# Performance work log

Measured on AMD Instinct MI355X. Metric: run time of the kernel, lower is better.

## Reference

```python
import jax, jax.numpy as jnp
import numpy as np

T, H, E, I, TOP_K = 4096, 1024, 8, 2048, 2
EPS = 1e-05


def setup_inputs() -> dict:
    key = jax.random.key(0)
    ks = jax.random.split(key, 4)
    x = jax.random.normal(ks[0], (T, H), dtype=jnp.float32)
    scale = jnp.ones((H,), dtype=jnp.float32)
    gate_kernel = jax.random.normal(ks[1], (H, E), dtype=jnp.float32) * (1.0 / np.sqrt(H))
    gate_bias = jnp.zeros((E,), dtype=jnp.float32)
    mlp1_weight = jax.random.normal(ks[2], (E, H, 2 * I), dtype=jnp.float32) * (1.0 / np.sqrt(H))
    mlp1_bias = jnp.zeros((E, 2 * I), dtype=jnp.float32)
    mlp2_weight = jax.random.normal(ks[3], (E, I, H), dtype=jnp.float32) * (1.0 / np.sqrt(I))
    mlp2_bias = jnp.zeros((E, H), dtype=jnp.float32)
    return {"x": x, "scale": scale, "gate_kernel": gate_kernel, "gate_bias": gate_bias,
            "mlp1_weight": mlp1_weight, "mlp1_bias": mlp1_bias,
            "mlp2_weight": mlp2_weight, "mlp2_bias": mlp2_bias}


def _rmsnorm(x, scale):
    t = x.astype(jnp.float32)
    rms = jnp.sqrt(jnp.mean(t * t, axis=-1, keepdims=True) + EPS)
    return ((t / rms) * scale).astype(x.dtype)


def reference(x, scale, gate_kernel, gate_bias, mlp1_weight, mlp1_bias, mlp2_weight, mlp2_bias):
    normed = _rmsnorm(x, scale)                                   # [T, H]
    _ = normed @ gate_kernel + gate_bias                          # gate logits (unused: static routing)
    # dense per-token, all-expert MLP: [T,H] x [E,H,2I] -> [T,E,2I]
    hidden = jnp.einsum('th,ehi->tei', normed, mlp1_weight) + mlp1_bias
    gate = jnp.minimum(hidden[..., :I], 7.0)
    linear = jnp.clip(hidden[..., I:], -7.0, 7.0)
    activated = gate * jax.nn.sigmoid(1.702 * gate) * (linear + 1.0)
    expert_out = jnp.einsum('tei,eih->teh', activated, mlp2_weight) + mlp2_bias  # [T,E,H]
    # static uniform routing over the first TOP_K experts
    mix = jnp.where(jnp.arange(E) < TOP_K, 1.0 / TOP_K, 0.0).astype(x.dtype)     # [E]
    fused = jnp.einsum('teh,e->th', expert_out, mix)
    return x + fused
```

## Files before the change

kernel.cpp:

```cpp
#include <hip/hip_runtime.h>
#include <hip/hip_bf16.h>
#include <stdint.h>

#define T_DIM 4096
#define H_DIM 1024
#define I_DIM 2048

typedef __bf16 bf16x8 __attribute__((ext_vector_type(8)));
typedef float f32x4 __attribute__((ext_vector_type(4)));
typedef unsigned short ushort_t;
typedef unsigned short us4 __attribute__((ext_vector_type(4)));

__device__ __forceinline__ unsigned short f32_to_bf16(float f) {
  unsigned int u = __float_as_uint(f);
  u += 0x7fffu + ((u >> 16) & 1u);
  return (unsigned short)(u >> 16);
}

__device__ __forceinline__ void gload_lds16(const void* g, void* l) {
  __builtin_amdgcn_global_load_lds(
      (__attribute__((address_space(1))) void*)(uintptr_t)g,
      (__attribute__((address_space(3))) void*)(unsigned int)(uintptr_t)l,
      16, 0, 0);
}

__device__ __forceinline__ int swz(int L) { return L ^ (((L >> 7) & 7) << 4); }

#define S_BARRIER() asm volatile("s_barrier" ::: "memory")
#define WAITV(n) asm volatile("s_waitcnt vmcnt(" #n ")" ::: "memory")
#define IRFENCE() asm volatile("" ::: "memory")
#define MFMA16(acc, va, vb) \
  acc = __builtin_amdgcn_mfma_f32_16x16x32_bf16(va, vb, acc, 0, 0, 0)

__global__ __launch_bounds__(256) void k_rmsnorm_init(
    const float* __restrict__ x, const float* __restrict__ scale,
    const float* __restrict__ b2, ushort_t* __restrict__ normed,
    float* __restrict__ out) {
  const int row = blockIdx.x, tid = threadIdx.x;
  const float4 v = ((const float4*)(x + (size_t)row * H_DIM))[tid];
  float ss = v.x * v.x + v.y * v.y + v.z * v.z + v.w * v.w;
#pragma unroll
  for (int off = 32; off > 0; off >>= 1) ss += __shfl_xor(ss, off);
  __shared__ float wsum[4];
  if ((tid & 63) == 0) wsum[tid >> 6] = ss;
  __syncthreads();
  const float tot = wsum[0] + wsum[1] + wsum[2] + wsum[3];
  const float inv = rsqrtf(tot * (1.0f / H_DIM) + 1e-5f);
  const float4 sc = ((const float4*)scale)[tid];
  us4 o;
  o.x = f32_to_bf16(v.x * inv * sc.x);
  o.y = f32_to_bf16(v.y * inv * sc.y);
  o.z = f32_to_bf16(v.z * inv * sc.z);
  o.w = f32_to_bf16(v.w * inv * sc.w);
  ((us4*)(normed + (size_t)row * H_DIM))[tid] = o;
  const float4 b0 = ((const float4*)b2)[tid];
  const float4 b1 = ((const float4*)(b2 + H_DIM))[tid];
  float4 ov;
  ov.x = v.x + 0.5f * (b0.x + b1.x);
  ov.y = v.y + 0.5f * (b0.y + b1.y);
  ov.z = v.z + 0.5f * (b0.z + b1.z);
  ov.w = v.w + 0.5f * (b0.w + b1.w);
  ((float4*)(out + (size_t)row * H_DIM))[tid] = ov;
}

__global__ __launch_bounds__(256) void k_transpose_cvt(const float* __restrict__ src,
                                                       ushort_t* __restrict__ dst,
                                                       int R, int C) {
  __shared__ float tile[32][33];
  const size_t eoff = (size_t)blockIdx.z * (size_t)R * (size_t)C;
  src += eoff;
  dst += eoff;
  const int x0 = blockIdx.x * 32, y0 = blockIdx.y * 32;
  const int tx = threadIdx.x & 31, ty = threadIdx.x >> 5;
#pragma unroll
  for (int i = 0; i < 4; ++i)
    tile[ty + 8 * i][tx] = src[(size_t)(y0 + ty + 8 * i) * C + x0 + tx];
  __syncthreads();
#pragma unroll
  for (int i = 0; i < 4; ++i)
    dst[(size_t)(x0 + ty + 8 * i) * R + y0 + tx] = f32_to_bf16(tile[tx][ty + 8 * i]);
}

__global__ __launch_bounds__(512, 2) void k_gemm1_8ph(
    const ushort_t* __restrict__ normed, const ushort_t* __restrict__ w1T,
    const float* __restrict__ b1, ushort_t* __restrict__ act) {
  __shared__ __align__(16) ushort_t lds[2][4][8192];
  char* const ldsB = (char*)&lds[0][0][0];
  const int tid = threadIdx.x;
  const int wg = (blockIdx.x & 7) * 64 + (blockIdx.x >> 3);
  const int e = wg >> 8;
  const int rem = wg & 255;
  const int brow = (rem >> 4) * 256;
  const int bcol = (rem & 15) * 128;
  const int lane = tid & 63;
  const int wm = (tid >> 6) >> 1;
  const int wn = (tid >> 6) & 1;
  const int r16 = lane & 15, kh = lane >> 4;

  const ushort_t* aBase = normed + (size_t)brow * H_DIM;
  const ushort_t* gBase = w1T + ((size_t)e * 2 * I_DIM + bcol) * H_DIM;
  const ushort_t* lBase = gBase + (size_t)I_DIM * H_DIM;

  f32x4 accg[4][4], accl[4][4];
  const f32x4 zf = {0.f, 0.f, 0.f, 0.f};
#pragma unroll
  for (int m = 0; m < 4; ++m)
#pragma unroll
    for (int n = 0; n < 4; ++n) { accg[m][n] = zf; accl[m][n] = zf; }

  int srow[2], scolb[2];
#pragma unroll
  for (int j = 0; j < 2; ++j) {
    const int u = swz((j * 512 + tid) * 16);
    srow[j] = u >> 6;
    scolb[j] = (u & 63) >> 1;
  }
  const int ldst0 = (tid & ~63) * 16;

  const ushort_t* pA0 = aBase + (size_t)srow[0] * H_DIM + scolb[0];
  const ushort_t* pA1 = aBase + (size_t)srow[1] * H_DIM + scolb[1];
  const ushort_t* pG = gBase + (size_t)srow[0] * H_DIM + scolb[0];
  const ushort_t* pL = lBase + (size_t)(srow[1] - 128) * H_DIM + scolb[1];

  int aoffV[2][4], boffV[2][4];
#pragma unroll
  for (int bq = 0; bq < 2; ++bq) {
#pragma unroll
    for (int m = 0; m < 4; ++m)
      aoffV[bq][m] = bq * 65536 + swz((wm * 64 + m * 16 + r16) * 64 + kh * 16);
#pragma unroll
    for (int n = 0; n < 4; ++n)
      boffV[bq][n] = bq * 65536 + 16384 + swz((wn * 64 + n * 16 + r16) * 64 + kh * 16);
  }

  auto stageA = [&](int buf, int ksub) {
    gload_lds16(pA0 + ksub * 32, ldsB + buf * 65536 + ksub * 32768 + ldst0);
    gload_lds16(pA1 + ksub * 32, ldsB + buf * 65536 + ksub * 32768 + 8192 + ldst0);
  };
  auto stageB = [&](int buf, int ksub) {
    gload_lds16(pG + ksub * 32, ldsB + buf * 65536 + ksub * 32768 + 16384 + ldst0);
    gload_lds16(pL + ksub * 32, ldsB + buf * 65536 + ksub * 32768 + 16384 + 8192 + ldst0);
  };
  auto rdA = [&](int buf, int ksub, int m) -> bf16x8 {
    return *(const bf16x8*)(ldsB + aoffV[buf][m] + ksub * 32768);
  };
  auto rdBg = [&](int buf, int ksub, int n) -> bf16x8 {
    return *(const bf16x8*)(ldsB + boffV[buf][n] + ksub * 32768);
  };
  auto rdBl = [&](int buf, int ksub, int n) -> bf16x8 {
    return *(const bf16x8*)(ldsB + boffV[buf][n] + ksub * 32768 + 8192);
  };

#define G1_ADV() \
  { pA0 += 64; pA1 += 64; pG += 64; pL += 64; }

#define G1_HALF(CUR, NXT, KS)                                                 \
  {                                                                           \
    _Pragma("unroll") for (int m = 0; m < 4; ++m) a[m] = rdA(CUR, KS, m);     \
    _Pragma("unroll") for (int n = 0; n < 4; ++n) b[n] = rdBg(CUR, KS, n);    \
    stageA(NXT, KS);                                                          \
    stageB(NXT, KS);                                                          \
    __builtin_amdgcn_s_setprio(1);                                            \
    _Pragma("unroll") for (int m = 0; m < 4; ++m)                             \
        _Pragma("unroll") for (int n = 0; n < 4; ++n)                         \
            MFMA16(accg[m][n], a[m], b[n]);                                   \
    __builtin_amdgcn_s_setprio(0);                                            \
    _Pragma("unroll") for (int n = 0; n < 4; ++n) b[n] = rdBl(CUR, KS, n);    \
    __builtin_amdgcn_s_setprio(1);                                            \
    _Pragma("unroll") for (int m = 0; m < 4; ++m)                             \
        _Pragma("unroll") for (int n = 0; n < 4; ++n)                         \
            MFMA16(accl[m][n], a[m], b[n]);                                   \
    __builtin_amdgcn_s_setprio(0);                                            \
    WAITV(4);                                                                 \
    S_BARRIER();                                                              \
  }

#define G1_TILE(CUR, NXT)  \
  { G1_HALF(CUR, NXT, 0); G1_HALF(CUR, NXT, 1); G1_ADV(); }

  stageA(0, 0); stageB(0, 0); IRFENCE();
  stageA(0, 1); stageB(0, 1);
  G1_ADV();
  WAITV(4);
  S_BARRIER();

  bf16x8 a[4], b[4];
#pragma unroll 1
  for (int it = 0; it < 7; ++it) {
    G1_TILE(0, 1);
    G1_TILE(1, 0);
  }
  G1_TILE(0, 1);

  {
#pragma unroll
    for (int m = 0; m < 4; ++m) a[m] = rdA(1, 0, m);
#pragma unroll
    for (int n = 0; n < 4; ++n) b[n] = rdBg(1, 0, n);
#pragma unroll
    for (int m = 0; m < 4; ++m)
#pragma unroll
      for (int n = 0; n < 4; ++n) MFMA16(accg[m][n], a[m], b[n]);
#pragma unroll
    for (int n = 0; n < 4; ++n) b[n] = rdBl(1, 0, n);
#pragma unroll
    for (int m = 0; m < 4; ++m)
#pragma unroll
      for (int n = 0; n < 4; ++n) MFMA16(accl[m][n], a[m], b[n]);
    WAITV(0);
    S_BARRIER();
#pragma unroll
    for (int m = 0; m < 4; ++m) a[m] = rdA(1, 1, m);
#pragma unroll
    for (int n = 0; n < 4; ++n) b[n] = rdBg(1, 1, n);
#pragma unroll
    for (int m = 0; m < 4; ++m)
#pragma unroll
      for (int n = 0; n < 4; ++n) MFMA16(accg[m][n], a[m], b[n]);
#pragma unroll
    for (int n = 0; n < 4; ++n) b[n] = rdBl(1, 1, n);
#pragma unroll
    for (int m = 0; m < 4; ++m)
#pragma unroll
      for (int n = 0; n < 4; ++n) MFMA16(accl[m][n], a[m], b[n]);
  }
#undef G1_HALF
#undef G1_TILE
#undef G1_ADV

  const float* b1e = b1 + (size_t)e * 2 * I_DIM;
#pragma unroll
  for (int m = 0; m < 4; ++m)
#pragma unroll
    for (int n = 0; n < 4; ++n) {
      const int gcol = bcol + wn * 64 + n * 16 + r16;
      const float bgb = b1e[gcol];
      const float blb = b1e[I_DIM + gcol];
#pragma unroll
      for (int rr = 0; rr < 4; ++rr) {
        const int grow = brow + wm * 64 + m * 16 + kh * 4 + rr;
        const float hg = accg[m][n][rr] + bgb;
        const float hl = accl[m][n][rr] + blb;
        const float g = fminf(hg, 7.f);
        const float l = fminf(fmaxf(hl, -7.f), 7.f);
        const float s = 1.f / (1.f + __expf(-1.702f * g));
        const float av = g * s * (l + 1.f);
        act[((size_t)e * T_DIM + grow) * I_DIM + gcol] = f32_to_bf16(av);
      }
    }
}

__global__ __launch_bounds__(512, 2) void k_gemm2_8ph(
    const ushort_t* __restrict__ act, const ushort_t* __restrict__ w2T,
    float* __restrict__ out) {
  __shared__ __align__(16) ushort_t lds[2][2][12288];
  char* const ldsB = (char*)&lds[0][0][0];
  const int tid = threadIdx.x;
  const int wg = (blockIdx.x & 7) * 32 + (blockIdx.x >> 3);
  const int e = wg >> 7;
  const int tileid = wg & 127;
  const int brow = (tileid >> 3) * 256;
  const int bcol = (tileid & 7) * 128;
  const int lane = tid & 63;
  const int wm = (tid >> 6) >> 1;
  const int wn = (tid >> 6) & 1;
  const int r16 = lane & 15, kh = lane >> 4;

  const ushort_t* aBase = act + ((size_t)e * T_DIM + brow) * I_DIM;
  const ushort_t* bBase = w2T + ((size_t)e * H_DIM + bcol) * I_DIM;

  f32x4 acc[4][4];
  const f32x4 zf = {0.f, 0.f, 0.f, 0.f};
#pragma unroll
  for (int m = 0; m < 4; ++m)
#pragma unroll
    for (int n = 0; n < 4; ++n) acc[m][n] = zf;

  int srow[2], scolb[2];
#pragma unroll
  for (int j = 0; j < 2; ++j) {
    const int u = swz((j * 512 + tid) * 16);
    srow[j] = u >> 6;
    scolb[j] = (u & 63) >> 1;
  }
  const int ldst0 = (tid & ~63) * 16;

  const ushort_t* pA0 = aBase + (size_t)srow[0] * I_DIM + scolb[0];
  const ushort_t* pA1 = aBase + (size_t)srow[1] * I_DIM + scolb[1];
  const ushort_t* pB = bBase + (size_t)srow[0] * I_DIM + scolb[0];

  int aoffV[2][4], boffV[2][4];
#pragma unroll
  for (int bq = 0; bq < 2; ++bq) {
#pragma unroll
    for (int m = 0; m < 4; ++m)
      aoffV[bq][m] = bq * 49152 + swz((wm * 64 + m * 16 + r16) * 64 + kh * 16);
#pragma unroll
    for (int n = 0; n < 4; ++n)
      boffV[bq][n] = bq * 49152 + 16384 + swz((wn * 64 + n * 16 + r16) * 64 + kh * 16);
  }

  auto stageA = [&](int buf, int ksub) {
    gload_lds16(pA0 + ksub * 32, ldsB + buf * 49152 + ksub * 24576 + ldst0);
    gload_lds16(pA1 + ksub * 32, ldsB + buf * 49152 + ksub * 24576 + 8192 + ldst0);
  };
  auto stageB = [&](int buf, int ksub) {
    gload_lds16(pB + ksub * 32, ldsB + buf * 49152 + ksub * 24576 + 16384 + ldst0);
  };
  auto rdA = [&](int buf, int ksub, int m) -> bf16x8 {
    return *(const bf16x8*)(ldsB + aoffV[buf][m] + ksub * 24576);
  };
  auto rdB = [&](int buf, int ksub, int n) -> bf16x8 {
    return *(const bf16x8*)(ldsB + boffV[buf][n] + ksub * 24576);
  };

#define G2_ADV() \
  { pA0 += 64; pA1 += 64; pB += 64; }

#define G2_HALF(CUR, NXT, KS)                                                 \
  {                                                                           \
    _Pragma("unroll") for (int m = 0; m < 4; ++m) a[m] = rdA(CUR, KS, m);     \
    _Pragma("unroll") for (int n = 0; n < 4; ++n) b[n] = rdB(CUR, KS, n);     \
    stageA(NXT, KS);                                                          \
    stageB(NXT, KS);                                                          \
    __builtin_amdgcn_s_setprio(1);                                            \
    _Pragma("unroll") for (int m = 0; m < 4; ++m)                             \
        _Pragma("unroll") for (int n = 0; n < 4; ++n)                         \
            MFMA16(acc[m][n], a[m], b[n]);                                    \
    __builtin_amdgcn_s_setprio(0);                                            \
    WAITV(3);                                                                 \
    S_BARRIER();                                                              \
  }

#define G2_TILE(CUR, NXT)  \
  { G2_HALF(CUR, NXT, 0); G2_HALF(CUR, NXT, 1); G2_ADV(); }

  stageA(0, 0); stageB(0, 0); IRFENCE();
  stageA(0, 1); stageB(0, 1);
  G2_ADV();
  WAITV(3);
  S_BARRIER();

  bf16x8 a[4], b[4];
#pragma unroll 1
  for (int it = 0; it < 15; ++it) {
    G2_TILE(0, 1);
    G2_TILE(1, 0);
  }
  G2_TILE(0, 1);

  {
#pragma unroll
    for (int m = 0; m < 4; ++m) a[m] = rdA(1, 0, m);
#pragma unroll
    for (int n = 0; n < 4; ++n) b[n] = rdB(1, 0, n);
#pragma unroll
    for (int m = 0; m < 4; ++m)
#pragma unroll
      for (int n = 0; n < 4; ++n) MFMA16(acc[m][n], a[m], b[n]);
    WAITV(0);
    S_BARRIER();
#pragma unroll
    for (int m = 0; m < 4; ++m) a[m] = rdA(1, 1, m);
#pragma unroll
    for (int n = 0; n < 4; ++n) b[n] = rdB(1, 1, n);
#pragma unroll
    for (int m = 0; m < 4; ++m)
#pragma unroll
      for (int n = 0; n < 4; ++n) MFMA16(acc[m][n], a[m], b[n]);
  }
#undef G2_HALF
#undef G2_TILE
#undef G2_ADV

#pragma unroll
  for (int m = 0; m < 4; ++m)
#pragma unroll
    for (int n = 0; n < 4; ++n) {
      const int gcol = bcol + wn * 64 + n * 16 + r16;
#pragma unroll
      for (int rr = 0; rr < 4; ++rr) {
        const int grow = brow + wm * 64 + m * 16 + kh * 4 + rr;
        atomicAdd(&out[(size_t)grow * H_DIM + gcol], 0.5f * acc[m][n][rr]);
      }
    }
}

extern "C" void kernel_launch(void* const* d_in, const int* in_sizes, int n_in,
                              void* d_out, int out_size, void* d_ws, size_t ws_size,
                              hipStream_t stream) {
  const float* x = (const float*)d_in[0];
  const float* scale = (const float*)d_in[1];
  const float* w1 = (const float*)d_in[4];
  const float* b1 = (const float*)d_in[5];
  const float* w2 = (const float*)d_in[6];
  const float* b2 = (const float*)d_in[7];
  float* out = (float*)d_out;

  ushort_t* ws = (ushort_t*)d_ws;
  ushort_t* normed = ws;
  ushort_t* w1T = normed + (size_t)T_DIM * H_DIM;
  ushort_t* w2T = w1T + (size_t)2 * 2 * I_DIM * H_DIM;
  ushort_t* actb = w2T + (size_t)2 * H_DIM * I_DIM;

  k_rmsnorm_init<<<dim3(T_DIM), 256, 0, stream>>>(x, scale, b2, normed, out);
  k_transpose_cvt<<<dim3(2 * I_DIM / 32, H_DIM / 32, 2), 256, 0, stream>>>(
      w1, w1T, H_DIM, 2 * I_DIM);
  k_transpose_cvt<<<dim3(H_DIM / 32, I_DIM / 32, 2), 256, 0, stream>>>(
      w2, w2T, I_DIM, H_DIM);
  k_gemm1_8ph<<<dim3(512), 512, 0, stream>>>(normed, w1T, b1, actb);
  k_gemm2_8ph<<<dim3(256), 512, 0, stream>>>(actb, w2T, out);
}
```

Before: 149.2 us.

## Load A operand directly from global into registers, stage only B via LDS

Both GEMM kernels stop staging the activation (A) tile through shared memory and instead have each wave load its A fragments straight from global memory into registers, in the MFMA fragment layout. Only the weight (B) tile is still double-buffered in LDS, which shrinks shared memory use and cuts LDS write/read traffic and wait counts. The trade-off is that A rows are re-fetched by every wave sharing them (wn=0/1), so global and L2 traffic goes up. The global loads also sit on the critical path with no prefetch ahead of the MFMAs, so memory latency may be exposed.

```diff
diff --git a/kernel.cpp b/kernel.cpp
--- a/kernel.cpp
+++ b/kernel.cpp
@@ -81,10 +81,10 @@
     dst[(size_t)(x0 + ty + 8 * i) * R + y0 + tx] = f32_to_bf16(tile[tx][ty + 8 * i]);
 }
 
-__global__ __launch_bounds__(512, 2) void k_gemm1_8ph(
+__global__ __launch_bounds__(512, 2) void k_gemm1(
     const ushort_t* __restrict__ normed, const ushort_t* __restrict__ w1T,
     const float* __restrict__ b1, ushort_t* __restrict__ act) {
-  __shared__ __align__(16) ushort_t lds[2][4][8192];
+  __shared__ __align__(16) ushort_t lds[2][2][8192];
   char* const ldsB = (char*)&lds[0][0][0];
   const int tid = threadIdx.x;
   const int wg = (blockIdx.x & 7) * 64 + (blockIdx.x >> 3);
@@ -97,7 +97,6 @@
   const int wn = (tid >> 6) & 1;
   const int r16 = lane & 15, kh = lane >> 4;
 
-  const ushort_t* aBase = normed + (size_t)brow * H_DIM;
   const ushort_t* gBase = w1T + ((size_t)e * 2 * I_DIM + bcol) * H_DIM;
   const ushort_t* lBase = gBase + (size_t)I_DIM * H_DIM;
 
@@ -117,48 +116,39 @@
   }
   const int ldst0 = (tid & ~63) * 16;
 
-  const ushort_t* pA0 = aBase + (size_t)srow[0] * H_DIM + scolb[0];
-  const ushort_t* pA1 = aBase + (size_t)srow[1] * H_DIM + scolb[1];
   const ushort_t* pG = gBase + (size_t)srow[0] * H_DIM + scolb[0];
   const ushort_t* pL = lBase + (size_t)(srow[1] - 128) * H_DIM + scolb[1];
-
-  int aoffV[2][4], boffV[2][4];
-#pragma unroll
-  for (int bq = 0; bq < 2; ++bq) {
-#pragma unroll
-    for (int m = 0; m < 4; ++m)
-      aoffV[bq][m] = bq * 65536 + swz((wm * 64 + m * 16 + r16) * 64 + kh * 16);
+  const ushort_t* pA = normed + (size_t)(brow + wm * 64 + r16) * H_DIM + kh * 8;
+
+  int boffV[2][4];
+#pragma unroll
+  for (int bq = 0; bq < 2; ++bq)
 #pragma unroll
     for (int n = 0; n < 4; ++n)
-      boffV[bq][n] = bq * 65536 + 16384 + swz((wn * 64 + n * 16 + r16) * 64 + kh * 16);
-  }
-
-  auto stageA = [&](int buf, int ksub) {
-    gload_lds16(pA0 + ksub * 32, ldsB + buf * 65536 + ksub * 32768 + ldst0);
-    gload_lds16(pA1 + ksub * 32, ldsB + buf * 65536 + ksub * 32768 + 8192 + ldst0);
-  };
+      boffV[bq][n] = bq * 32768 + swz((wn * 64 + n * 16 + r16) * 64 + kh * 16);
+
   auto stageB = [&](int buf, int ksub) {
-    gload_lds16(pG + ksub * 32, ldsB + buf * 65536 + ksub * 32768 + 16384 + ldst0);
-    gload_lds16(pL + ksub * 32, ldsB + buf * 65536 + ksub * 32768 + 16384 + 8192 + ldst0);
-  };
-  auto rdA = [&](int buf, int ksub, int m) -> bf16x8 {
-    return *(const bf16x8*)(ldsB + aoffV[buf][m] + ksub * 32768);
+    gload_lds16(pG + ksub * 32, ldsB + buf * 32768 + ksub * 16384 + ldst0);
+    gload_lds16(pL + ksub * 32, ldsB + buf * 32768 + ksub * 16384 + 8192 + ldst0);
   };
   auto rdBg = [&](int buf, int ksub, int n) -> bf16x8 {
-    return *(const bf16x8*)(ldsB + boffV[buf][n] + ksub * 32768);
+    return *(const bf16x8*)(ldsB + boffV[buf][n] + ksub * 16384);
   };
   auto rdBl = [&](int buf, int ksub, int n) -> bf16x8 {
-    return *(const bf16x8*)(ldsB + boffV[buf][n] + ksub * 32768 + 8192);
+    return *(const bf16x8*)(ldsB + boffV[buf][n] + ksub * 16384 + 8192);
+  };
+  auto ldA = [&](int ksub, int m) -> bf16x8 {
+    return *(const bf16x8*)(pA + (size_t)m * 16 * H_DIM + ksub * 32);
   };
 
 #define G1_ADV() \
-  { pA0 += 64; pA1 += 64; pG += 64; pL += 64; }
+  { pA += 64; pG += 64; pL += 64; }
 
 #define G1_HALF(CUR, NXT, KS)                                                 \
   {                                                                           \
-    _Pragma("unroll") for (int m = 0; m < 4; ++m) a[m] = rdA(CUR, KS, m);     \
+    _Pragma("unroll") for (int m = 0; m < 4; ++m) a[m] = ldA(KS, m);          \
+    IRFENCE();                                                                \
     _Pragma("unroll") for (int n = 0; n < 4; ++n) b[n] = rdBg(CUR, KS, n);    \
-    stageA(NXT, KS);                                                          \
     stageB(NXT, KS);                                                          \
     __builtin_amdgcn_s_setprio(1);                                            \
     _Pragma("unroll") for (int m = 0; m < 4; ++m)                             \
@@ -171,17 +161,17 @@
         _Pragma("unroll") for (int n = 0; n < 4; ++n)                         \
             MFMA16(accl[m][n], a[m], b[n]);                                   \
     __builtin_amdgcn_s_setprio(0);                                            \
-    WAITV(4);                                                                 \
+    WAITV(2);                                                                 \
     S_BARRIER();                                                              \
   }
 
 #define G1_TILE(CUR, NXT)  \
   { G1_HALF(CUR, NXT, 0); G1_HALF(CUR, NXT, 1); G1_ADV(); }
 
-  stageA(0, 0); stageB(0, 0); IRFENCE();
-  stageA(0, 1); stageB(0, 1);
-  G1_ADV();
-  WAITV(4);
+  stageB(0, 0); IRFENCE();
+  stageB(0, 1);
+  pG += 64; pL += 64;
+  WAITV(2);
   S_BARRIER();
 
   bf16x8 a[4], b[4];
@@ -194,7 +184,7 @@
 
   {
 #pragma unroll
-    for (int m = 0; m < 4; ++m) a[m] = rdA(1, 0, m);
+    for (int m = 0; m < 4; ++m) a[m] = ldA(0, m);
 #pragma unroll
     for (int n = 0; n < 4; ++n) b[n] = rdBg(1, 0, n);
 #pragma unroll
@@ -210,7 +200,7 @@
     WAITV(0);
     S_BARRIER();
 #pragma unroll
-    for (int m = 0; m < 4; ++m) a[m] = rdA(1, 1, m);
+    for (int m = 0; m < 4; ++m) a[m] = ldA(1, m);
 #pragma unroll
     for (int n = 0; n < 4; ++n) b[n] = rdBg(1, 1, n);
 #pragma unroll
@@ -250,10 +240,10 @@
     }
 }
 
-__global__ __launch_bounds__(512, 2) void k_gemm2_8ph(
+__global__ __launch_bounds__(512, 2) void k_gemm2(
     const ushort_t* __restrict__ act, const ushort_t* __restrict__ w2T,
     float* __restrict__ out) {
-  __shared__ __align__(16) ushort_t lds[2][2][12288];
+  __shared__ __align__(16) ushort_t lds[2][2][4096];
   char* const ldsB = (char*)&lds[0][0][0];
   const int tid = threadIdx.x;
   const int wg = (blockIdx.x & 7) * 32 + (blockIdx.x >> 3);
@@ -266,7 +256,6 @@
   const int wn = (tid >> 6) & 1;
   const int r16 = lane & 15, kh = lane >> 4;
 
-  const ushort_t* aBase = act + ((size_t)e * T_DIM + brow) * I_DIM;
   const ushort_t* bBase = w2T + ((size_t)e * H_DIM + bcol) * I_DIM;
 
   f32x4 acc[4][4];
@@ -276,69 +265,56 @@
 #pragma unroll
     for (int n = 0; n < 4; ++n) acc[m][n] = zf;
 
-  int srow[2], scolb[2];
-#pragma unroll
-  for (int j = 0; j < 2; ++j) {
-    const int u = swz((j * 512 + tid) * 16);
-    srow[j] = u >> 6;
-    scolb[j] = (u & 63) >> 1;
-  }
+  const int u0 = swz(tid * 16);
+  const int srow0 = u0 >> 6;
+  const int scolb0 = (u0 & 63) >> 1;
   const int ldst0 = (tid & ~63) * 16;
 
-  const ushort_t* pA0 = aBase + (size_t)srow[0] * I_DIM + scolb[0];
-  const ushort_t* pA1 = aBase + (size_t)srow[1] * I_DIM + scolb[1];
-  const ushort_t* pB = bBase + (size_t)srow[0] * I_DIM + scolb[0];
-
-  int aoffV[2][4], boffV[2][4];
-#pragma unroll
-  for (int bq = 0; bq < 2; ++bq) {
-#pragma unroll
-    for (int m = 0; m < 4; ++m)
-      aoffV[bq][m] = bq * 49152 + swz((wm * 64 + m * 16 + r16) * 64 + kh * 16);
+  const ushort_t* pB = bBase + (size_t)srow0 * I_DIM + scolb0;
+  const ushort_t* pA = act + ((size_t)e * T_DIM + brow + wm * 64 + r16) * I_DIM + kh * 8;
+
+  int boffV[2][4];
+#pragma unroll
+  for (int bq = 0; bq < 2; ++bq)
 #pragma unroll
     for (int n = 0; n < 4; ++n)
-      boffV[bq][n] = bq * 49152 + 16384 + swz((wn * 64 + n * 16 + r16) * 64 + kh * 16);
-  }
-
-  auto stageA = [&](int buf, int ksub) {
-    gload_lds16(pA0 + ksub * 32, ldsB + buf * 49152 + ksub * 24576 + ldst0);
-    gload_lds16(pA1 + ksub * 32, ldsB + buf * 49152 + ksub * 24576 + 8192 + ldst0);
-  };
+      boffV[bq][n] = bq * 16384 + swz((wn * 64 + n * 16 + r16) * 64 + kh * 16);
+
   auto stageB = [&](int buf, int ksub) {
-    gload_lds16(pB + ksub * 32, ldsB + buf * 49152 + ksub * 24576 + 16384 + ldst0);
-  };
-  auto rdA = [&](int buf, int ksub, int m) -> bf16x8 {
-    return *(const bf16x8*)(ldsB + aoffV[buf][m] + ksub * 24576);
+    gload_lds16(pB + ksub * 32, ldsB + buf * 16384 + ksub * 8192 + ldst0);
   };
   auto rdB = [&](int buf, int ksub, int n) -> bf16x8 {
-    return *(const bf16x8*)(ldsB + boffV[buf][n] + ksub * 24576);
+    return *(const bf16x8*)(ldsB + boffV[buf][n] + ksub * 8192);
+  };
+  auto ldA = [&](int ksub, int m) -> bf16x8 {
+    return *(const bf16x8*)(pA + (size_t)m * 16 * I_DIM + ksub * 32);
   };
 
 #define G2_ADV() \
-  { pA0 += 64; pA1 += 64; pB += 64; }
+  { pA += 64; pB += 64; }
 
 #define G2_HALF(CUR, NXT, KS)                                                 \
   {                                                                           \
-    _Pragma("unroll") for (int m = 0; m < 4; ++m) a[m] = rdA(CUR, KS, m);     \
+    _Pragma("unroll") for (int m = 0; m < 4; ++m) a[m] = ldA(KS, m);          \
+    IRFENCE();                                                                \
     _Pragma("unroll") for (int n = 0; n < 4; ++n) b[n] = rdB(CUR, KS, n);     \
-    stageA(NXT, KS);                                                          \
     stageB(NXT, KS);                                                          \
     __builtin_amdgcn_s_setprio(1);                                            \
     _Pragma("unroll") for (int m = 0; m < 4; ++m)                             \
         _Pragma("unroll") for (int n = 0; n < 4; ++n)                         \
             MFMA16(acc[m][n], a[m], b[n]);                                    \
     __builtin_amdgcn_s_setprio(0);                                            \
-    WAITV(3);                                                                 \
+    WAITV(1);                                                                 \
     S_BARRIER();                                                              \
   }
 
 #define G2_TILE(CUR, NXT)  \
   { G2_HALF(CUR, NXT, 0); G2_HALF(CUR, NXT, 1); G2_ADV(); }
 
-  stageA(0, 0); stageB(0, 0); IRFENCE();
-  stageA(0, 1); stageB(0, 1);
-  G2_ADV();
-  WAITV(3);
+  stageB(0, 0); IRFENCE();
+  stageB(0, 1);
+  pB += 64;
+  WAITV(1);
   S_BARRIER();
 
   bf16x8 a[4], b[4];
@@ -351,7 +327,7 @@
 
   {
 #pragma unroll
-    for (int m = 0; m < 4; ++m) a[m] = rdA(1, 0, m);
+    for (int m = 0; m < 4; ++m) a[m] = ldA(0, m);
 #pragma unroll
     for (int n = 0; n < 4; ++n) b[n] = rdB(1, 0, n);
 #pragma unroll
@@ -361,7 +337,7 @@
     WAITV(0);
     S_BARRIER();
 #pragma unroll
-    for (int m = 0; m < 4; ++m) a[m] = rdA(1, 1, m);
+    for (int m = 0; m < 4; ++m) a[m] = ldA(1, m);
 #pragma unroll
     for (int n = 0; n < 4; ++n) b[n] = rdB(1, 1, n);
 #pragma unroll
@@ -408,6 +384,6 @@
       w1, w1T, H_DIM, 2 * I_DIM);
   k_transpose_cvt<<<dim3(H_DIM / 32, I_DIM / 32, 2), 256, 0, stream>>>(
       w2, w2T, I_DIM, H_DIM);
-  k_gemm1_8ph<<<dim3(512), 512, 0, stream>>>(normed, w1T, b1, actb);
-  k_gemm2_8ph<<<dim3(256), 512, 0, stream>>>(actb, w2T, out);
-}
+  k_gemm1<<<dim3(512), 512, 0, stream>>>(normed, w1T, b1, actb);
+  k_gemm2<<<dim3(256), 512, 0, stream>>>(actb, w2T, out);
+}
```

New measurement: 240.5 us. 1.61x slower.

## Remap GEMM waves to 2x4 layout and split k-steps into barrier-synchronized phases

Applied to the files above, without the earlier changes.

Both expert GEMM kernels change their wave layout from 4x2 (64x64 per wave) to 2x4 (128x32 per wave). Each k-half is split into two MFMA phases, each preceded by LDS fragment reads, issuing only the A or B global-to-LDS stage. Phases are fenced with s_barrier, lgkmcnt(0) waits and sched_barrier. The aim is an 8-phase, ping-pong style schedule that interleaves memory and MFMA work across waves and keeps B fragments resident. The cost is more barriers per iteration and more A-fragment LDS reads per wave.

```diff
diff --git a/kernel.cpp b/kernel.cpp
--- a/kernel.cpp
+++ b/kernel.cpp
@@ -28,6 +28,8 @@
 
 #define S_BARRIER() asm volatile("s_barrier" ::: "memory")
 #define WAITV(n) asm volatile("s_waitcnt vmcnt(" #n ")" ::: "memory")
+#define LGKM0() asm volatile("s_waitcnt lgkmcnt(0)" ::: "memory")
+#define SCHEDB() __builtin_amdgcn_sched_barrier(0)
 #define IRFENCE() asm volatile("" ::: "memory")
 #define MFMA16(acc, va, vb) \
   acc = __builtin_amdgcn_mfma_f32_16x16x32_bf16(va, vb, acc, 0, 0, 0)
@@ -81,7 +83,7 @@
     dst[(size_t)(x0 + ty + 8 * i) * R + y0 + tx] = f32_to_bf16(tile[tx][ty + 8 * i]);
 }
 
-__global__ __launch_bounds__(512, 2) void k_gemm1_8ph(
+__global__ __launch_bounds__(512, 2) void k_gemm1(
     const ushort_t* __restrict__ normed, const ushort_t* __restrict__ w1T,
     const float* __restrict__ b1, ushort_t* __restrict__ act) {
   __shared__ __align__(16) ushort_t lds[2][4][8192];
@@ -93,20 +95,20 @@
   const int brow = (rem >> 4) * 256;
   const int bcol = (rem & 15) * 128;
   const int lane = tid & 63;
-  const int wm = (tid >> 6) >> 1;
-  const int wn = (tid >> 6) & 1;
+  const int wid = tid >> 6;
+  const int wm = wid >> 2;
+  const int wn = wid & 3;
   const int r16 = lane & 15, kh = lane >> 4;
 
-  const ushort_t* aBase = normed + (size_t)brow * H_DIM;
   const ushort_t* gBase = w1T + ((size_t)e * 2 * I_DIM + bcol) * H_DIM;
   const ushort_t* lBase = gBase + (size_t)I_DIM * H_DIM;
 
-  f32x4 accg[4][4], accl[4][4];
+  f32x4 accg[8][2], accl[8][2];
   const f32x4 zf = {0.f, 0.f, 0.f, 0.f};
 #pragma unroll
-  for (int m = 0; m < 4; ++m)
-#pragma unroll
-    for (int n = 0; n < 4; ++n) { accg[m][n] = zf; accl[m][n] = zf; }
+  for (int m = 0; m < 8; ++m)
+#pragma unroll
+    for (int n = 0; n < 2; ++n) { accg[m][n] = zf; accl[m][n] = zf; }
 
   int srow[2], scolb[2];
 #pragma unroll
@@ -117,66 +119,75 @@
   }
   const int ldst0 = (tid & ~63) * 16;
 
-  const ushort_t* pA0 = aBase + (size_t)srow[0] * H_DIM + scolb[0];
-  const ushort_t* pA1 = aBase + (size_t)srow[1] * H_DIM + scolb[1];
+  const ushort_t* pA0 = normed + (size_t)(brow + srow[0]) * H_DIM + scolb[0];
+  const ushort_t* pA1 = normed + (size_t)(brow + srow[1]) * H_DIM + scolb[1];
   const ushort_t* pG = gBase + (size_t)srow[0] * H_DIM + scolb[0];
   const ushort_t* pL = lBase + (size_t)(srow[1] - 128) * H_DIM + scolb[1];
 
-  int aoffV[2][4], boffV[2][4];
-#pragma unroll
-  for (int bq = 0; bq < 2; ++bq) {
-#pragma unroll
-    for (int m = 0; m < 4; ++m)
-      aoffV[bq][m] = bq * 65536 + swz((wm * 64 + m * 16 + r16) * 64 + kh * 16);
-#pragma unroll
-    for (int n = 0; n < 4; ++n)
-      boffV[bq][n] = bq * 65536 + 16384 + swz((wn * 64 + n * 16 + r16) * 64 + kh * 16);
-  }
-
-  auto stageA = [&](int buf, int ksub) {
-    gload_lds16(pA0 + ksub * 32, ldsB + buf * 65536 + ksub * 32768 + ldst0);
-    gload_lds16(pA1 + ksub * 32, ldsB + buf * 65536 + ksub * 32768 + 8192 + ldst0);
+  int avo[2], bvo[2];
+  {
+    const int abase = swz((wm * 128 + r16) * 64 + kh * 16);
+    const int bbase = 16384 + swz((wn * 32 + r16) * 64 + kh * 16);
+#pragma unroll
+    for (int bq = 0; bq < 2; ++bq) {
+      avo[bq] = bq * 65536 + abase;
+      bvo[bq] = bq * 65536 + bbase;
+    }
+  }
+
+  auto stageA = [&](int buf, int ks) {
+    gload_lds16(pA0 + ks * 32, ldsB + buf * 65536 + ks * 32768 + ldst0);
+    gload_lds16(pA1 + ks * 32, ldsB + buf * 65536 + ks * 32768 + 8192 + ldst0);
   };
-  auto stageB = [&](int buf, int ksub) {
-    gload_lds16(pG + ksub * 32, ldsB + buf * 65536 + ksub * 32768 + 16384 + ldst0);
-    gload_lds16(pL + ksub * 32, ldsB + buf * 65536 + ksub * 32768 + 16384 + 8192 + ldst0);
-  };
-  auto rdA = [&](int buf, int ksub, int m) -> bf16x8 {
-    return *(const bf16x8*)(ldsB + aoffV[buf][m] + ksub * 32768);
-  };
-  auto rdBg = [&](int buf, int ksub, int n) -> bf16x8 {
-    return *(const bf16x8*)(ldsB + boffV[buf][n] + ksub * 32768);
-  };
-  auto rdBl = [&](int buf, int ksub, int n) -> bf16x8 {
-    return *(const bf16x8*)(ldsB + boffV[buf][n] + ksub * 32768 + 8192);
+  auto stageB = [&](int buf, int ks) {
+    gload_lds16(pG + ks * 32, ldsB + buf * 65536 + ks * 32768 + 16384 + ldst0);
+    gload_lds16(pL + ks * 32, ldsB + buf * 65536 + ks * 32768 + 16384 + 8192 + ldst0);
   };
 
 #define G1_ADV() \
   { pA0 += 64; pA1 += 64; pG += 64; pL += 64; }
 
-#define G1_HALF(CUR, NXT, KS)                                                 \
+#define G1_KHALF(C, N, KS)                                                    \
   {                                                                           \
-    _Pragma("unroll") for (int m = 0; m < 4; ++m) a[m] = rdA(CUR, KS, m);     \
-    _Pragma("unroll") for (int n = 0; n < 4; ++n) b[n] = rdBg(CUR, KS, n);    \
-    stageA(NXT, KS);                                                          \
-    stageB(NXT, KS);                                                          \
+    _Pragma("unroll") for (int m = 0; m < 4; ++m)                             \
+        a[m] = *(const bf16x8*)(ldsB + avo[C] + KS * 32768 + m * 1024);       \
+    _Pragma("unroll") for (int n = 0; n < 2; ++n) {                           \
+      bg[n] = *(const bf16x8*)(ldsB + bvo[C] + KS * 32768 + n * 1024);        \
+      bl[n] = *(const bf16x8*)(ldsB + bvo[C] + KS * 32768 + 8192 + n * 1024); \
+    }                                                                         \
+    stageA(N, KS);                                                            \
+    S_BARRIER();                                                              \
+    LGKM0();                                                                  \
+    SCHEDB();                                                                 \
     __builtin_amdgcn_s_setprio(1);                                            \
     _Pragma("unroll") for (int m = 0; m < 4; ++m)                             \
-        _Pragma("unroll") for (int n = 0; n < 4; ++n)                         \
-            MFMA16(accg[m][n], a[m], b[n]);                                   \
+        _Pragma("unroll") for (int n = 0; n < 2; ++n) {                       \
+      MFMA16(accg[m][n], a[m], bg[n]);                                        \
+      MFMA16(accl[m][n], a[m], bl[n]);                                        \
+    }                                                                         \
     __builtin_amdgcn_s_setprio(0);                                            \
-    _Pragma("unroll") for (int n = 0; n < 4; ++n) b[n] = rdBl(CUR, KS, n);    \
+    S_BARRIER();                                                              \
+    SCHEDB();                                                                 \
+    _Pragma("unroll") for (int m = 0; m < 4; ++m)                             \
+        a[m] = *(const bf16x8*)(ldsB + avo[C] + KS * 32768 + 4096 + m * 1024);\
+    stageB(N, KS);                                                            \
+    S_BARRIER();                                                              \
+    LGKM0();                                                                  \
+    SCHEDB();                                                                 \
     __builtin_amdgcn_s_setprio(1);                                            \
     _Pragma("unroll") for (int m = 0; m < 4; ++m)                             \
-        _Pragma("unroll") for (int n = 0; n < 4; ++n)                         \
-            MFMA16(accl[m][n], a[m], b[n]);                                   \
+        _Pragma("unroll") for (int n = 0; n < 2; ++n) {                       \
+      MFMA16(accg[m + 4][n], a[m], bg[n]);                                    \
+      MFMA16(accl[m + 4][n], a[m], bl[n]);                                    \
+    }                                                                         \
     __builtin_amdgcn_s_setprio(0);                                            \
     WAITV(4);                                                                 \
     S_BARRIER();                                                              \
-  }
-
-#define G1_TILE(CUR, NXT)  \
-  { G1_HALF(CUR, NXT, 0); G1_HALF(CUR, NXT, 1); G1_ADV(); }
+    SCHEDB();                                                                 \
+  }
+
+#define G1_TILE(C, N)  \
+  { G1_KHALF(C, N, 0); G1_KHALF(C, N, 1); G1_ADV(); }
 
   stageA(0, 0); stageB(0, 0); IRFENCE();
   stageA(0, 1); stageB(0, 1);
@@ -184,7 +195,7 @@
   WAITV(4);
   S_BARRIER();
 
-  bf16x8 a[4], b[4];
+  bf16x8 a[4], bg[2], bl[2];
 #pragma unroll 1
   for (int it = 0; it < 7; ++it) {
     G1_TILE(0, 1);
@@ -194,51 +205,73 @@
 
   {
 #pragma unroll
-    for (int m = 0; m < 4; ++m) a[m] = rdA(1, 0, m);
-#pragma unroll
-    for (int n = 0; n < 4; ++n) b[n] = rdBg(1, 0, n);
-#pragma unroll
-    for (int m = 0; m < 4; ++m)
-#pragma unroll
-      for (int n = 0; n < 4; ++n) MFMA16(accg[m][n], a[m], b[n]);
-#pragma unroll
-    for (int n = 0; n < 4; ++n) b[n] = rdBl(1, 0, n);
-#pragma unroll
-    for (int m = 0; m < 4; ++m)
-#pragma unroll
-      for (int n = 0; n < 4; ++n) MFMA16(accl[m][n], a[m], b[n]);
+    for (int m = 0; m < 4; ++m)
+      a[m] = *(const bf16x8*)(ldsB + avo[1] + m * 1024);
+#pragma unroll
+    for (int n = 0; n < 2; ++n) {
+      bg[n] = *(const bf16x8*)(ldsB + bvo[1] + n * 1024);
+      bl[n] = *(const bf16x8*)(ldsB + bvo[1] + 8192 + n * 1024);
+    }
+#pragma unroll
+    for (int m = 0; m < 4; ++m)
+#pragma unroll
+      for (int n = 0; n < 2; ++n) {
+        MFMA16(accg[m][n], a[m], bg[n]);
+        MFMA16(accl[m][n], a[m], bl[n]);
+      }
+#pragma unroll
+    for (int m = 0; m < 4; ++m)
+      a[m] = *(const bf16x8*)(ldsB + avo[1] + 4096 + m * 1024);
+#pragma unroll
+    for (int m = 0; m < 4; ++m)
+#pragma unroll
+      for (int n = 0; n < 2; ++n) {
+        MFMA16(accg[m + 4][n], a[m], bg[n]);
+        MFMA16(accl[m + 4][n], a[m], bl[n]);
+      }
     WAITV(0);
     S_BARRIER();
 #pragma unroll
-    for (int m = 0; m < 4; ++m) a[m] = rdA(1, 1, m);
-#pragma unroll
-    for (int n = 0; n < 4; ++n) b[n] = rdBg(1, 1, n);
-#pragma unroll
-    for (int m = 0; m < 4; ++m)
-#pragma unroll
-      for (int n = 0; n < 4; ++n) MFMA16(accg[m][n], a[m], b[n]);
-#pragma unroll
-    for (int n = 0; n < 4; ++n) b[n] = rdBl(1, 1, n);
-#pragma unroll
-    for (int m = 0; m < 4; ++m)
-#pragma unroll
-      for (int n = 0; n < 4; ++n) MFMA16(accl[m][n], a[m], b[n]);
-  }
-#undef G1_HALF
+    for (int m = 0; m < 4; ++m)
+      a[m] = *(const bf16x8*)(ldsB + avo[1] + 32768 + m * 1024);
+#pragma unroll
+    for (int n = 0; n < 2; ++n) {
+      bg[n] = *(const bf16x8*)(ldsB + bvo[1] + 32768 + n * 1024);
+      bl[n] = *(const bf16x8*)(ldsB + bvo[1] + 32768 + 8192 + n * 1024);
+    }
+#pragma unroll
+    for (int m = 0; m < 4; ++m)
+#pragma unroll
+      for (int n = 0; n < 2; ++n) {
+        MFMA16(accg[m][n], a[m], bg[n]);
+        MFMA16(accl[m][n], a[m], bl[n]);
+      }
+#pragma unroll
+    for (int m = 0; m < 4; ++m)
+      a[m] = *(const bf16x8*)(ldsB + avo[1] + 32768 + 4096 + m * 1024);
+#pragma unroll
+    for (int m = 0; m < 4; ++m)
+#pragma unroll
+      for (int n = 0; n < 2; ++n) {
+        MFMA16(accg[m + 4][n], a[m], bg[n]);
+        MFMA16(accl[m + 4][n], a[m], bl[n]);
+      }
+  }
+#undef G1_KHALF
 #undef G1_TILE
 #undef G1_ADV
 
   const float* b1e = b1 + (size_t)e * 2 * I_DIM;
 #pragma unroll
-  for (int m = 0; m < 4; ++m)
-#pragma unroll
-    for (int n = 0; n < 4; ++n) {
-      const int gcol = bcol + wn * 64 + n * 16 + r16;
+  for (int m = 0; m < 8; ++m)
+#pragma unroll
+    for (int n = 0; n < 2; ++n) {
+      const int gcol = bcol + wn * 32 + n * 16 + r16;
       const float bgb = b1e[gcol];
       const float blb = b1e[I_DIM + gcol];
 #pragma unroll
       for (int rr = 0; rr < 4; ++rr) {
-        const int grow = brow + wm * 64 + m * 16 + kh * 4 + rr;
+        const int grow = brow + wm * 128 + m * 16 + kh * 4 + rr;
         const float hg = accg[m][n][rr] + bgb;
         const float hl = accl[m][n][rr] + blb;
         const float g = fminf(hg, 7.f);
@@ -250,7 +283,7 @@
     }
 }
 
-__global__ __launch_bounds__(512, 2) void k_gemm2_8ph(
+__global__ __launch_bounds__(512, 2) void k_gemm2(
     const ushort_t* __restrict__ act, const ushort_t* __restrict__ w2T,
     float* __restrict__ out) {
   __shared__ __align__(16) ushort_t lds[2][2][12288];
@@ -262,19 +295,20 @@
   const int brow = (tileid >> 3) * 256;
   const int bcol = (tileid & 7) * 128;
   const int lane = tid & 63;
-  const int wm = (tid >> 6) >> 1;
-  const int wn = (tid >> 6) & 1;
+  const int wid = tid >> 6;
+  const int wm = wid >> 2;
+  const int wn = wid & 3;
   const int r16 = lane & 15, kh = lane >> 4;
 
   const ushort_t* aBase = act + ((size_t)e * T_DIM + brow) * I_DIM;
   const ushort_t* bBase = w2T + ((size_t)e * H_DIM + bcol) * I_DIM;
 
-  f32x4 acc[4][4];
+  f32x4 acc[8][2];
   const f32x4 zf = {0.f, 0.f, 0.f, 0.f};
 #pragma unroll
-  for (int m = 0; m < 4; ++m)
-#pragma unroll
-    for (int n = 0; n < 4; ++n) acc[m][n] = zf;
+  for (int m = 0; m < 8; ++m)
+#pragma unroll
+    for (int n = 0; n < 2; ++n) acc[m][n] = zf;
 
   int srow[2], scolb[2];
 #pragma unroll
@@ -289,51 +323,63 @@
   const ushort_t* pA1 = aBase + (size_t)srow[1] * I_DIM + scolb[1];
   const ushort_t* pB = bBase + (size_t)srow[0] * I_DIM + scolb[0];
 
-  int aoffV[2][4], boffV[2][4];
-#pragma unroll
-  for (int bq = 0; bq < 2; ++bq) {
-#pragma unroll
-    for (int m = 0; m < 4; ++m)
-      aoffV[bq][m] = bq * 49152 + swz((wm * 64 + m * 16 + r16) * 64 + kh * 16);
-#pragma unroll
-    for (int n = 0; n < 4; ++n)
-      boffV[bq][n] = bq * 49152 + 16384 + swz((wn * 64 + n * 16 + r16) * 64 + kh * 16);
-  }
-
-  auto stageA = [&](int buf, int ksub) {
-    gload_lds16(pA0 + ksub * 32, ldsB + buf * 49152 + ksub * 24576 + ldst0);
-    gload_lds16(pA1 + ksub * 32, ldsB + buf * 49152 + ksub * 24576 + 8192 + ldst0);
+  int avo[2], bvo[2];
+  {
+    const int abase = swz((wm * 128 + r16) * 64 + kh * 16);
+    const int bbase = 16384 + swz((wn * 32 + r16) * 64 + kh * 16);
+#pragma unroll
+    for (int bq = 0; bq < 2; ++bq) {
+      avo[bq] = bq * 49152 + abase;
+      bvo[bq] = bq * 49152 + bbase;
+    }
+  }
+
+  auto stageA = [&](int buf, int ks) {
+    gload_lds16(pA0 + ks * 32, ldsB + buf * 49152 + ks * 24576 + ldst0);
+    gload_lds16(pA1 + ks * 32, ldsB + buf * 49152 + ks * 24576 + 8192 + ldst0);
   };
-  auto stageB = [&](int buf, int ksub) {
-    gload_lds16(pB + ksub * 32, ldsB + buf * 49152 + ksub * 24576 + 16384 + ldst0);
-  };
-  auto rdA = [&](int buf, int ksub, int m) -> bf16x8 {
-    return *(const bf16x8*)(ldsB + aoffV[buf][m] + ksub * 24576);
-  };
-  auto rdB = [&](int buf, int ksub, int n) -> bf16x8 {
-    return *(const bf16x8*)(ldsB + boffV[buf][n] + ksub * 24576);
+  auto stageB = [&](int buf, int ks) {
+    gload_lds16(pB + ks * 32, ldsB + buf * 49152 + ks * 24576 + 16384 + ldst0);
   };
 
 #define G2_ADV() \
   { pA0 += 64; pA1 += 64; pB += 64; }
 
-#define G2_HALF(CUR, NXT, KS)                                                 \
+#define G2_KHALF(C, N, KS)                                                    \
   {                                                                           \
-    _Pragma("unroll") for (int m = 0; m < 4; ++m) a[m] = rdA(CUR, KS, m);     \
-    _Pragma("unroll") for (int n = 0; n < 4; ++n) b[n] = rdB(CUR, KS, n);     \
-    stageA(NXT, KS);                                                          \
-    stageB(NXT, KS);                                                          \
+    _Pragma("unroll") for (int m = 0; m < 4; ++m)                             \
+        a[m] = *(const bf16x8*)(ldsB + avo[C] + KS * 24576 + m * 1024);       \
+    _Pragma("unroll") for (int n = 0; n < 2; ++n)                             \
+        b[n] = *(const bf16x8*)(ldsB + bvo[C] + KS * 24576 + n * 1024);       \
+    stageA(N, KS);                                                            \
+    S_BARRIER();                                                              \
+    LGKM0();                                                                  \
+    SCHEDB();                                                                 \
     __builtin_amdgcn_s_setprio(1);                                            \
     _Pragma("unroll") for (int m = 0; m < 4; ++m)                             \
-        _Pragma("unroll") for (int n = 0; n < 4; ++n)                         \
+        _Pragma("unroll") for (int n = 0; n < 2; ++n)                         \
             MFMA16(acc[m][n], a[m], b[n]);                                    \
     __builtin_amdgcn_s_setprio(0);                                            \
+    S_BARRIER();                                                              \
+    SCHEDB();                                                                 \
+    _Pragma("unroll") for (int m = 0; m < 4; ++m)                             \
+        a[m] = *(const bf16x8*)(ldsB + avo[C] + KS * 24576 + 4096 + m * 1024);\
+    stageB(N, KS);                                                            \
+    S_BARRIER();                                                              \
+    LGKM0();                                                                  \
+    SCHEDB();                                                                 \
+    __builtin_amdgcn_s_setprio(1);                                            \
+    _Pragma("unroll") for (int m = 0; m < 4; ++m)                             \
+        _Pragma("unroll") for (int n = 0; n < 2; ++n)                         \
+            MFMA16(acc[m + 4][n], a[m], b[n]);                                \
+    __builtin_amdgcn_s_setprio(0);                                            \
     WAITV(3);                                                                 \
     S_BARRIER();                                                              \
-  }
-
-#define G2_TILE(CUR, NXT)  \
-  { G2_HALF(CUR, NXT, 0); G2_HALF(CUR, NXT, 1); G2_ADV(); }
+    SCHEDB();                                                                 \
+  }
+
+#define G2_TILE(C, N)  \
+  { G2_KHALF(C, N, 0); G2_KHALF(C, N, 1); G2_ADV(); }
 
   stageA(0, 0); stageB(0, 0); IRFENCE();
   stageA(0, 1); stageB(0, 1);
@@ -341,7 +387,7 @@
   WAITV(3);
   S_BARRIER();
 
-  bf16x8 a[4], b[4];
+  bf16x8 a[4], b[2];
 #pragma unroll 1
   for (int it = 0; it < 15; ++it) {
     G2_TILE(0, 1);
@@ -351,36 +397,54 @@
 
   {
 #pragma unroll
-    for (int m = 0; m < 4; ++m) a[m] = rdA(1, 0, m);
-#pragma unroll
-    for (int n = 0; n < 4; ++n) b[n] = rdB(1, 0, n);
-#pragma unroll
-    for (int m = 0; m < 4; ++m)
-#pragma unroll
-      for (int n = 0; n < 4; ++n) MFMA16(acc[m][n], a[m], b[n]);
+    for (int m = 0; m < 4; ++m)
+      a[m] = *(const bf16x8*)(ldsB + avo[1] + m * 1024);
+#pragma unroll
+    for (int n = 0; n < 2; ++n)
+      b[n] = *(const bf16x8*)(ldsB + bvo[1] + n * 1024);
+#pragma unroll
+    for (int m = 0; m < 4; ++m)
+#pragma unroll
+      for (int n = 0; n < 2; ++n) MFMA16(acc[m][n], a[m], b[n]);
+#pragma unroll
+    for (int m = 0; m < 4; ++m)
+      a[m] = *(const bf16x8*)(ldsB + avo[1] + 4096 + m * 1024);
+#pragma unroll
+    for (int m = 0; m < 4; ++m)
+#pragma unroll
+      for (int n = 0; n < 2; ++n) MFMA16(acc[m + 4][n], a[m], b[n]);
     WAITV(0);
     S_BARRIER();
 #pragma unroll
-    for (int m = 0; m < 4; ++m) a[m] = rdA(1, 1, m);
-#pragma unroll
-    for (int n = 0; n < 4; ++n) b[n] = rdB(1, 1, n);
-#pragma unroll
-    for (int m = 0; m < 4; ++m)
-#pragma unroll
-      for (int n = 0; n < 4; ++n) MFMA16(acc[m][n], a[m], b[n]);
-  }
-#undef G2_HALF
+    for (int m = 0; m < 4; ++m)
+      a[m] = *(const bf16x8*)(ldsB + avo[1] + 24576 + m * 1024);
+#pragma unroll
+    for (int n = 0; n < 2; ++n)
+      b[n] = *(const bf16x8*)(ldsB + bvo[1] + 24576 + n * 1024);
+#pragma unroll
+    for (int m = 0; m < 4; ++m)
+#pragma unroll
+      for (int n = 0; n < 2; ++n) MFMA16(acc[m][n], a[m], b[n]);
+#pragma unroll
+    for (int m = 0; m < 4; ++m)
+      a[m] = *(const bf16x8*)(ldsB + avo[1] + 24576 + 4096 + m * 1024);
+#pragma unroll
+    for (int m = 0; m < 4; ++m)
+#pragma unroll
+      for (int n = 0; n < 2; ++n) MFMA16(acc[m + 4][n], a[m], b[n]);
+  }
+#undef G2_KHALF
 #undef G2_TILE
 #undef G2_ADV
 
 #pragma unroll
-  for (int m = 0; m < 4; ++m)
-#pragma unroll
-    for (int n = 0; n < 4; ++n) {
-      const int gcol = bcol + wn * 64 + n * 16 + r16;
+  for (int m = 0; m < 8; ++m)
+#pragma unroll
+    for (int n = 0; n < 2; ++n) {
+      const int gcol = bcol + wn * 32 + n * 16 + r16;
 #pragma unroll
       for (int rr = 0; rr < 4; ++rr) {
-        const int grow = brow + wm * 64 + m * 16 + kh * 4 + rr;
+        const int grow = brow + wm * 128 + m * 16 + kh * 4 + rr;
         atomicAdd(&out[(size_t)grow * H_DIM + gcol], 0.5f * acc[m][n][rr]);
       }
     }
@@ -408,6 +472,6 @@
       w1, w1T, H_DIM, 2 * I_DIM);
   k_transpose_cvt<<<dim3(H_DIM / 32, I_DIM / 32, 2), 256, 0, stream>>>(
       w2, w2T, I_DIM, H_DIM);
-  k_gemm1_8ph<<<dim3(512), 512, 0, stream>>>(normed, w1T, b1, actb);
-  k_gemm2_8ph<<<dim3(256), 512, 0, stream>>>(actb, w2T, out);
-}
+  k_gemm1<<<dim3(512), 512, 0, stream>>>(normed, w1T, b1, actb);
+  k_gemm2<<<dim3(256), 512, 0, stream>>>(actb, w2T, out);
+}
```

New measurement: 153.4 us. 1.03x slower.
